# Kernel tuning notes

Hardware: AMD Instinct MI355X
Metric: run time of the kernel (lower is better)

Reference implementation:

```python
import jax, jax.numpy as jnp
import numpy as np

B, N, C = 2, 2048, 768
H = 12
HD = C // H  # 64


def setup_inputs() -> dict:
    key = jax.random.key(0)
    ks = jax.random.split(key, 6)
    s = 0.02
    x = jax.random.normal(ks[0], (B, N, C), dtype=jnp.float32)
    xpos = jnp.arange(B * N, dtype=jnp.int64).reshape(B, N) % N
    W_qkv = jax.random.normal(ks[1], (3 * C, C), dtype=jnp.float32) * s
    b_qkv = jnp.zeros((3 * C,), dtype=jnp.float32)
    W_proj = jax.random.normal(ks[2], (C, C), dtype=jnp.float32) * s
    b_proj = jnp.zeros((C,), dtype=jnp.float32)
    return {"x": x, "xpos": xpos, "W_qkv": W_qkv, "b_qkv": b_qkv,
            "W_proj": W_proj, "b_proj": b_proj}


def reference(x, xpos, W_qkv, b_qkv, W_proj, b_proj):
    # rope is None in this configuration -> xpos is unused, matching torch module.
    Bx, Nx, Cx = x.shape
    scale = (Cx // H) ** -0.5
    qkv = x @ W_qkv.T + b_qkv                     # [B, N, 3C]
    qkv = qkv.reshape(Bx, Nx, 3, H, HD)
    q = jnp.einsum('bnhd->bhnd', qkv[:, :, 0])    # [B, H, N, HD]
    k = jnp.einsum('bnhd->bhnd', qkv[:, :, 1])
    v = jnp.einsum('bnhd->bhnd', qkv[:, :, 2])
    attn = jnp.einsum('bhnd,bhmd->bhnm', q, k) * scale  # [B, H, N, N]
    attn = jax.nn.softmax(attn, axis=-1)
    out = jnp.einsum('bhnm,bhmd->bhnd', attn, v)  # [B, H, N, HD]
    out = jnp.einsum('bhnd->bnhd', out).reshape(Bx, Nx, Cx)
    return out @ W_proj.T + b_proj
```

## Files before the change

kernel.cpp:

```cpp
#include <hip/hip_runtime.h>
#include <hip/hip_bf16.h>


typedef _Float16 half8 __attribute__((ext_vector_type(8)));
typedef _Float16 half4_t __attribute__((ext_vector_type(4)));
typedef float floatx4 __attribute__((ext_vector_type(4)));
typedef float floatx16 __attribute__((ext_vector_type(16)));
typedef unsigned int uintx4 __attribute__((ext_vector_type(4)));
typedef unsigned int uintx2 __attribute__((ext_vector_type(2)));

#define SCALE_LOG2E 0.1803368801111204f

constexpr int XH_OFF    = 0;
constexpr int WQKV_OFF  = XH_OFF + 4096 * 768;
constexpr int WPROJ_OFF = WQKV_OFF + 2304 * 768;
constexpr int QK_OFF    = WPROJ_OFF + 768 * 768;
constexpr int VTH_OFF   = QK_OFF + 4096 * 1536;
constexpr int PO_OFF    = VTH_OFF + 24 * 64 * 2048;
constexpr int PSTAT_OFF = PO_OFF + 2 * 24 * 2048 * 64;

__device__ __forceinline__ void gl16(const _Float16* g, _Float16* l) {
  __builtin_amdgcn_global_load_lds(
      (const __attribute__((address_space(1))) unsigned int*)g,
      (__attribute__((address_space(3))) unsigned int*)l, 16, 0, 0);
}

__global__ __launch_bounds__(256) void cvt_all(const float* __restrict__ x,
                                               const float* __restrict__ wqkv,
                                               const float* __restrict__ wproj,
                                               _Float16* __restrict__ ws) {
  constexpr int n1 = 4096 * 768 / 4;
  constexpr int n2 = 2304 * 768 / 4;
  int i = blockIdx.x * 256 + threadIdx.x;
  const float* src; _Float16* dst; int j;
  if (i < n1)           { src = x;     dst = ws + XH_OFF;    j = i; }
  else if (i < n1 + n2) { src = wqkv;  dst = ws + WQKV_OFF;  j = i - n1; }
  else                  { src = wproj; dst = ws + WPROJ_OFF; j = i - n1 - n2; }
  floatx4 f = *(const floatx4*)(src + 4 * j);
  half4_t h;
  h[0] = (_Float16)f[0]; h[1] = (_Float16)f[1];
  h[2] = (_Float16)f[2]; h[3] = (_Float16)f[3];
  *(half4_t*)(dst + 4 * j) = h;
}

__global__ __launch_bounds__(256) void qkv_gemm(const _Float16* __restrict__ xh,
                                                const _Float16* __restrict__ wh,
                                                const float* __restrict__ bias,
                                                _Float16* __restrict__ qkh,
                                                _Float16* __restrict__ vth) {
  __shared__ __align__(16) _Float16 sA[64 * 64];
  __shared__ __align__(16) _Float16 sB[128 * 64];
  const int tid = threadIdx.x;
  const int nblk = blockIdx.x % 18, mblk = blockIdx.x / 18;
  const int lane = tid & 63, w = tid >> 6;
  const int lane15 = lane & 15, quad = lane >> 4;
  const int lrow = lane >> 3, lchunk = lane & 7;

  floatx4 acc[4][2];
#pragma unroll
  for (int mt = 0; mt < 4; ++mt)
#pragma unroll
    for (int nt = 0; nt < 2; ++nt) acc[mt][nt] = (floatx4){0.f, 0.f, 0.f, 0.f};

  for (int kt = 0; kt < 12; ++kt) {
    if (kt) __syncthreads();
#pragma unroll
    for (int i = 0; i < 6; ++i) {
      int g = w * 48 + 8 * i;
      if (g < 64)
        gl16(xh + (mblk * 64 + g + lrow) * 768 + kt * 64 + lchunk * 8, sA + g * 64);
      else
        gl16(wh + (nblk * 128 + (g - 64) + lrow) * 768 + kt * 64 + lchunk * 8,
             sB + (g - 64) * 64);
    }
    __syncthreads();
#pragma unroll
    for (int ks = 0; ks < 2; ++ks) {
      half8 af[4], bf[2];
#pragma unroll
      for (int mt = 0; mt < 4; ++mt)
        af[mt] = *(const half8*)(sA + (mt * 16 + lane15) * 64 + ks * 32 + quad * 8);
#pragma unroll
      for (int nt = 0; nt < 2; ++nt)
        bf[nt] = *(const half8*)(sB + (w * 32 + nt * 16 + lane15) * 64 + ks * 32 + quad * 8);
#pragma unroll
      for (int mt = 0; mt < 4; ++mt)
#pragma unroll
        for (int nt = 0; nt < 2; ++nt)
          acc[mt][nt] = __builtin_amdgcn_mfma_f32_16x16x32_f16(af[mt], bf[nt], acc[mt][nt], 0, 0, 0);
    }
  }

  const int mbase = mblk * 64;
#pragma unroll
  for (int nt = 0; nt < 2; ++nt) {
    int cbase = nblk * 128 + w * 32 + nt * 16;
    float bv = bias[cbase + lane15];
    if (cbase < 1536) {
      int col = cbase + lane15;
      float sc = (cbase < 768) ? SCALE_LOG2E : 1.0f;
#pragma unroll
      for (int mt = 0; mt < 4; ++mt)
#pragma unroll
        for (int r = 0; r < 4; ++r) {
          int token = mbase + mt * 16 + quad * 4 + r;
          qkh[token * 1536 + col] = (_Float16)((acc[mt][nt][r] + bv) * sc);
        }
    } else {
      int dcol = cbase - 1536 + lane15;
      int h = dcol >> 6, d = dcol & 63;
#pragma unroll
      for (int mt = 0; mt < 4; ++mt) {
        int tok0 = mbase + mt * 16 + quad * 4;
        int b = tok0 >> 11, n0 = tok0 & 2047;
        int bh = b * 12 + h;
        half4_t hv;
#pragma unroll
        for (int r = 0; r < 4; ++r) hv[r] = (_Float16)(acc[mt][nt][r] + bv);
        *(half4_t*)(vth + (bh * 64 + d) * 2048 + n0) = hv;
      }
    }
  }
}

__global__ __launch_bounds__(256, 3) void attn_fused(const _Float16* __restrict__ qkh,
                                                     const _Float16* __restrict__ vth,
                                                     _Float16* __restrict__ pO,
                                                     float* __restrict__ pL) {
  __shared__ __align__(16) _Float16 sK[2][64 * 64];
  __shared__ __align__(16) _Float16 sVT[2][64 * 64];
  const int tid = threadIdx.x;
  const int bx = blockIdx.x;
  const int bh = bx % 24;
  const int rest = bx / 24;
  const int ks = rest & 1, qt = rest >> 1;
  const int b = bh / 12, h = bh % 12;
  const int lane = tid & 63, w = tid >> 6;
  const int q = lane & 31, hi = lane >> 5;

  const int qkbase = b * 2048 * 1536 + h * 64;
  const int qrow = qt * 128 + w * 32 + q;

  half8 qf[4];
#pragma unroll
  for (int c = 0; c < 4; ++c)
    qf[c] = *(const half8*)(qkh + qkbase + qrow * 1536 + c * 16 + hi * 8);

  const int srow = tid >> 2, sc = tid & 3;
  const int key0 = ks * 1024;
  const _Float16* kp = qkh + qkbase + 768 + (key0 + srow) * 1536 + sc * 8;
  const _Float16* vp = vth + (bh * 64 + srow) * 2048 + key0 + sc * 8;
  const int sw0 = srow * 64 + ((sc ^ (srow & 7)) * 8);
  const int sw1 = srow * 64 + (((sc + 4) ^ (srow & 7)) * 8);

  floatx16 O[2];
#pragma unroll
  for (int dg = 0; dg < 2; ++dg)
#pragma unroll
    for (int i = 0; i < 16; ++i) O[dg][i] = 0.f;
  float lrow = 0.f;

  half8 rk0 = *(const half8*)kp, rk1 = *(const half8*)(kp + 32);
  half8 rv0 = *(const half8*)vp, rv1 = *(const half8*)(vp + 32);
  kp += 64 * 1536; vp += 64;
  { _Float16* nK = &sK[0][0]; _Float16* nV = &sVT[0][0];
    *(half8*)(nK + sw0) = rk0; *(half8*)(nK + sw1) = rk1;
    *(half8*)(nV + sw0) = rv0; *(half8*)(nV + sw1) = rv1; }
  rk0 = *(const half8*)kp; rk1 = *(const half8*)(kp + 32);
  rv0 = *(const half8*)vp; rv1 = *(const half8*)(vp + 32);
  kp += 64 * 1536; vp += 64;

  for (int kt = 0; kt < 16; ++kt) {
    __syncthreads();
    const _Float16* cK = &sK[kt & 1][0];
    const _Float16* cV = &sVT[kt & 1][0];
    if (kt < 15) {
      _Float16* nK = &sK[(kt + 1) & 1][0];
      _Float16* nV = &sVT[(kt + 1) & 1][0];
      *(half8*)(nK + sw0) = rk0; *(half8*)(nK + sw1) = rk1;
      *(half8*)(nV + sw0) = rv0; *(half8*)(nV + sw1) = rv1;
      if (kt < 14) {
        rk0 = *(const half8*)kp; rk1 = *(const half8*)(kp + 32);
        rv0 = *(const half8*)vp; rv1 = *(const half8*)(vp + 32);
        kp += 64 * 1536; vp += 64;
      }
    }

    floatx16 s[2];
#pragma unroll
    for (int og = 0; og < 2; ++og)
#pragma unroll
      for (int i = 0; i < 16; ++i) s[og][i] = 0.f;
#pragma unroll
    for (int c = 0; c < 4; ++c) {
      const int rc = c * 2 + hi;
#pragma unroll
      for (int og = 0; og < 2; ++og) {
        const int krow = og * 32 + q;
        half8 kf = *(const half8*)(cK + krow * 64 + ((rc ^ (krow & 7)) * 8));
        s[og] = __builtin_amdgcn_mfma_f32_32x32x16_f16(kf, qf[c], s[og], 0, 0, 0);
      }
    }

    float p[2][16];
    float rsum = 0.f;
#pragma unroll
    for (int og = 0; og < 2; ++og)
#pragma unroll
      for (int r = 0; r < 16; ++r) {
        float e = exp2f(fminf(s[og][r], 30.f));
        p[og][r] = e;
        rsum += e;
      }
    lrow += rsum;

    half8 bfrag[4];
#pragma unroll
    for (int m = 0; m < 4; ++m) {
      const int og = m >> 1, rb = (m & 1) * 8;
      unsigned ua = __builtin_bit_cast(unsigned,
          __builtin_amdgcn_cvt_pkrtz(p[og][rb + 0], p[og][rb + 1]));
      unsigned ub = __builtin_bit_cast(unsigned,
          __builtin_amdgcn_cvt_pkrtz(p[og][rb + 2], p[og][rb + 3]));
      unsigned uc = __builtin_bit_cast(unsigned,
          __builtin_amdgcn_cvt_pkrtz(p[og][rb + 4], p[og][rb + 5]));
      unsigned ud = __builtin_bit_cast(unsigned,
          __builtin_amdgcn_cvt_pkrtz(p[og][rb + 6], p[og][rb + 7]));
      uintx2 sAC = __builtin_amdgcn_permlane32_swap(ua, uc, false, false);
      uintx2 sBD = __builtin_amdgcn_permlane32_swap(ub, ud, false, false);
      uintx4 u; u[0] = sAC[0]; u[1] = sBD[0]; u[2] = sAC[1]; u[3] = sBD[1];
      bfrag[m] = __builtin_bit_cast(half8, u);
    }

#pragma unroll
    for (int m = 0; m < 4; ++m) {
      const int rc2 = m * 2 + hi;
#pragma unroll
      for (int dg = 0; dg < 2; ++dg) {
        const int vrow = dg * 32 + q;
        half8 vf = *(const half8*)(cV + vrow * 64 + ((rc2 ^ (vrow & 7)) * 8));
        O[dg] = __builtin_amdgcn_mfma_f32_32x32x16_f16(vf, bfrag[m], O[dg], 0, 0, 0);
      }
    }
  }

  const int prow = (ks * 24 + bh) * 2048 + qt * 128 + w * 32;
#pragma unroll
  for (int dg = 0; dg < 2; ++dg)
#pragma unroll
    for (int g2 = 0; g2 < 4; ++g2) {
      half4_t hv;
#pragma unroll
      for (int e = 0; e < 4; ++e) hv[e] = (_Float16)O[dg][g2 * 4 + e];
      *(half4_t*)(pO + (prow + q) * 64 + dg * 32 + g2 * 8 + hi * 4) = hv;
    }
  lrow += __shfl_xor(lrow, 32, 64);
  if (lane < 32) pL[prow + lane] = lrow;
}

__global__ __launch_bounds__(256) void proj_gemm(const _Float16* __restrict__ pO,
                                                 const float* __restrict__ pL,
                                                 const _Float16* __restrict__ wh,
                                                 const float* __restrict__ bias,
                                                 float* __restrict__ out) {
  __shared__ __align__(16) _Float16 sA[64 * 72];
  __shared__ __align__(16) _Float16 sB[128 * 64];
  const int tid = threadIdx.x;
  const int nblk = blockIdx.x % 6, mblk = blockIdx.x / 6;
  const int lane = tid & 63, w = tid >> 6;
  const int lane15 = lane & 15, quad = lane >> 4;
  const int lrow = lane >> 3, lchunk = lane & 7;
  const int arow = tid >> 2, achk = tid & 3;
  const int tok0 = mblk * 64;
  const int b = tok0 >> 11, tokl = tok0 & 2047;

  floatx4 acc[4][2];
#pragma unroll
  for (int mt = 0; mt < 4; ++mt)
#pragma unroll
    for (int nt = 0; nt < 2; ++nt) acc[mt][nt] = (floatx4){0.f, 0.f, 0.f, 0.f};

  for (int kt = 0; kt < 12; ++kt) {
    const int bh = b * 12 + kt;
    const int row1 = bh * 2048 + tokl + arow;
    const int row2 = (24 + bh) * 2048 + tokl + arow;
    float f = 1.0f / (pL[row1] + pL[row2]);

    if (kt) __syncthreads();
#pragma unroll
    for (int i = 0; i < 4; ++i) {
      int g = w * 32 + 8 * i;
      gl16(wh + (nblk * 128 + g + lrow) * 768 + kt * 64 + lchunk * 8, sB + g * 64);
    }
#pragma unroll
    for (int cc = 0; cc < 2; ++cc) {
      int c8 = achk + 4 * cc;
      half8 o1 = *(const half8*)(pO + row1 * 64 + c8 * 8);
      half8 o2 = *(const half8*)(pO + row2 * 64 + c8 * 8);
      half8 o;
#pragma unroll
      for (int e = 0; e < 8; ++e)
        o[e] = (_Float16)(f * ((float)o1[e] + (float)o2[e]));
      *(half8*)(sA + arow * 72 + c8 * 8) = o;
    }
    __syncthreads();

#pragma unroll
    for (int ksplit = 0; ksplit < 2; ++ksplit) {
      half8 af[4], bf[2];
#pragma unroll
      for (int mt = 0; mt < 4; ++mt)
        af[mt] = *(const half8*)(sA + (mt * 16 + lane15) * 72 + ksplit * 32 + quad * 8);
#pragma unroll
      for (int nt = 0; nt < 2; ++nt)
        bf[nt] = *(const half8*)(sB + (w * 32 + nt * 16 + lane15) * 64 + ksplit * 32 + quad * 8);
#pragma unroll
      for (int mt = 0; mt < 4; ++mt)
#pragma unroll
        for (int nt = 0; nt < 2; ++nt)
          acc[mt][nt] = __builtin_amdgcn_mfma_f32_16x16x32_f16(af[mt], bf[nt], acc[mt][nt], 0, 0, 0);
    }
  }

  const int mbase = mblk * 64;
#pragma unroll
  for (int nt = 0; nt < 2; ++nt) {
    int col = nblk * 128 + w * 32 + nt * 16 + lane15;
    float bv = bias[col];
#pragma unroll
    for (int mt = 0; mt < 4; ++mt)
#pragma unroll
      for (int r = 0; r < 4; ++r) {
        int token = mbase + mt * 16 + quad * 4 + r;
        out[token * 768 + col] = acc[mt][nt][r] + bv;
      }
  }
}

extern "C" void kernel_launch(void* const* d_in, const int* in_sizes, int n_in,
                              void* d_out, int out_size, void* d_ws, size_t ws_size,
                              hipStream_t stream) {
  const float* x     = (const float*)d_in[0];
  const float* wqkv  = (const float*)d_in[2];
  const float* bqkv  = (const float*)d_in[3];
  const float* wproj = (const float*)d_in[4];
  const float* bproj = (const float*)d_in[5];
  float* out = (float*)d_out;

  _Float16* ws = (_Float16*)d_ws;
  _Float16* xh     = ws + XH_OFF;
  _Float16* wqkvh  = ws + WQKV_OFF;
  _Float16* wprojh = ws + WPROJ_OFF;
  _Float16* qkh    = ws + QK_OFF;
  _Float16* vth    = ws + VTH_OFF;
  _Float16* pO     = ws + PO_OFF;
  float*    pL     = (float*)(ws + PSTAT_OFF);

  constexpr int total_v4 = (4096 * 768 + 2304 * 768 + 768 * 768) / 4;
  cvt_all<<<total_v4 / 256, 256, 0, stream>>>(x, wqkv, wproj, ws);
  qkv_gemm<<<64 * 18, 256, 0, stream>>>(xh, wqkvh, bqkv, qkh, vth);
  attn_fused<<<24 * 32, 256, 0, stream>>>(qkh, vth, pO, pL);
  proj_gemm<<<64 * 6, 256, 0, stream>>>(pO, pL, wprojh, bproj, out);
}
```

Before: 183.0 us.

## Split attention keys four ways and enlarge QKV GEMM tiles to 128x128

The attention kernel is templated on the number of key splits. When the workspace is large enough it uses four key segments instead of two, doubling the block count to 1536 for better occupancy across CUs, and the projection GEMM sums all partial outputs and row sums. Separately, the QKV GEMM tile grows from 64x128 to 128x128, with each warp computing a 64x64 sub-tile, for more reuse per LDS load and fewer blocks. The costs are more partial-output traffic and merge work in the projection, and higher register pressure in the QKV GEMM.

```diff
diff --git a/kernel.cpp b/kernel.cpp
--- a/kernel.cpp
+++ b/kernel.cpp
@@ -17,7 +17,8 @@
 constexpr int QK_OFF    = WPROJ_OFF + 768 * 768;
 constexpr int VTH_OFF   = QK_OFF + 4096 * 1536;
 constexpr int PO_OFF    = VTH_OFF + 24 * 64 * 2048;
-constexpr int PSTAT_OFF = PO_OFF + 2 * 24 * 2048 * 64;
+constexpr size_t WS4_BYTES =
+    ((size_t)PO_OFF + (size_t)4 * 24 * 2048 * 64 + (size_t)4 * 24 * 2048 * 2) * 2;
 
 __device__ __forceinline__ void gl16(const _Float16* g, _Float16* l) {
   __builtin_amdgcn_global_load_lds(
@@ -48,53 +49,54 @@
                                                 const float* __restrict__ bias,
                                                 _Float16* __restrict__ qkh,
                                                 _Float16* __restrict__ vth) {
-  __shared__ __align__(16) _Float16 sA[64 * 64];
+  __shared__ __align__(16) _Float16 sA[128 * 64];
   __shared__ __align__(16) _Float16 sB[128 * 64];
   const int tid = threadIdx.x;
   const int nblk = blockIdx.x % 18, mblk = blockIdx.x / 18;
   const int lane = tid & 63, w = tid >> 6;
   const int lane15 = lane & 15, quad = lane >> 4;
   const int lrow = lane >> 3, lchunk = lane & 7;
-
-  floatx4 acc[4][2];
+  const int wq = w >> 1, wn = w & 1;
+
+  floatx4 acc[4][4];
 #pragma unroll
   for (int mt = 0; mt < 4; ++mt)
 #pragma unroll
-    for (int nt = 0; nt < 2; ++nt) acc[mt][nt] = (floatx4){0.f, 0.f, 0.f, 0.f};
+    for (int nt = 0; nt < 4; ++nt) acc[mt][nt] = (floatx4){0.f, 0.f, 0.f, 0.f};
 
   for (int kt = 0; kt < 12; ++kt) {
     if (kt) __syncthreads();
 #pragma unroll
-    for (int i = 0; i < 6; ++i) {
-      int g = w * 48 + 8 * i;
-      if (g < 64)
-        gl16(xh + (mblk * 64 + g + lrow) * 768 + kt * 64 + lchunk * 8, sA + g * 64);
+    for (int i = 0; i < 8; ++i) {
+      int g = i * 32 + w * 8;
+      if (g < 128)
+        gl16(xh + (mblk * 128 + g + lrow) * 768 + kt * 64 + lchunk * 8, sA + g * 64);
       else
-        gl16(wh + (nblk * 128 + (g - 64) + lrow) * 768 + kt * 64 + lchunk * 8,
-             sB + (g - 64) * 64);
+        gl16(wh + (nblk * 128 + (g - 128) + lrow) * 768 + kt * 64 + lchunk * 8,
+             sB + (g - 128) * 64);
     }
     __syncthreads();
 #pragma unroll
     for (int ks = 0; ks < 2; ++ks) {
-      half8 af[4], bf[2];
-#pragma unroll
-      for (int mt = 0; mt < 4; ++mt)
-        af[mt] = *(const half8*)(sA + (mt * 16 + lane15) * 64 + ks * 32 + quad * 8);
-#pragma unroll
-      for (int nt = 0; nt < 2; ++nt)
-        bf[nt] = *(const half8*)(sB + (w * 32 + nt * 16 + lane15) * 64 + ks * 32 + quad * 8);
-#pragma unroll
-      for (int mt = 0; mt < 4; ++mt)
-#pragma unroll
-        for (int nt = 0; nt < 2; ++nt)
+      half8 af[4], bf[4];
+#pragma unroll
+      for (int mt = 0; mt < 4; ++mt)
+        af[mt] = *(const half8*)(sA + (wq * 64 + mt * 16 + lane15) * 64 + ks * 32 + quad * 8);
+#pragma unroll
+      for (int nt = 0; nt < 4; ++nt)
+        bf[nt] = *(const half8*)(sB + (wn * 64 + nt * 16 + lane15) * 64 + ks * 32 + quad * 8);
+#pragma unroll
+      for (int mt = 0; mt < 4; ++mt)
+#pragma unroll
+        for (int nt = 0; nt < 4; ++nt)
           acc[mt][nt] = __builtin_amdgcn_mfma_f32_16x16x32_f16(af[mt], bf[nt], acc[mt][nt], 0, 0, 0);
     }
   }
 
-  const int mbase = mblk * 64;
-#pragma unroll
-  for (int nt = 0; nt < 2; ++nt) {
-    int cbase = nblk * 128 + w * 32 + nt * 16;
+  const int mbase = mblk * 128 + wq * 64;
+#pragma unroll
+  for (int nt = 0; nt < 4; ++nt) {
+    int cbase = nblk * 128 + wn * 64 + nt * 16;
     float bv = bias[cbase + lane15];
     if (cbase < 1536) {
       int col = cbase + lane15;
@@ -123,17 +125,20 @@
   }
 }
 
+template <int NKS>
 __global__ __launch_bounds__(256, 3) void attn_fused(const _Float16* __restrict__ qkh,
                                                      const _Float16* __restrict__ vth,
                                                      _Float16* __restrict__ pO,
                                                      float* __restrict__ pL) {
+  constexpr int SEG = 2048 / NKS;
+  constexpr int NT = SEG / 64;
   __shared__ __align__(16) _Float16 sK[2][64 * 64];
   __shared__ __align__(16) _Float16 sVT[2][64 * 64];
   const int tid = threadIdx.x;
   const int bx = blockIdx.x;
   const int bh = bx % 24;
   const int rest = bx / 24;
-  const int ks = rest & 1, qt = rest >> 1;
+  const int ks = rest % NKS, qt = rest / NKS;
   const int b = bh / 12, h = bh % 12;
   const int lane = tid & 63, w = tid >> 6;
   const int q = lane & 31, hi = lane >> 5;
@@ -147,7 +152,7 @@
     qf[c] = *(const half8*)(qkh + qkbase + qrow * 1536 + c * 16 + hi * 8);
 
   const int srow = tid >> 2, sc = tid & 3;
-  const int key0 = ks * 1024;
+  const int key0 = ks * SEG;
   const _Float16* kp = qkh + qkbase + 768 + (key0 + srow) * 1536 + sc * 8;
   const _Float16* vp = vth + (bh * 64 + srow) * 2048 + key0 + sc * 8;
   const int sw0 = srow * 64 + ((sc ^ (srow & 7)) * 8);
@@ -170,16 +175,16 @@
   rv0 = *(const half8*)vp; rv1 = *(const half8*)(vp + 32);
   kp += 64 * 1536; vp += 64;
 
-  for (int kt = 0; kt < 16; ++kt) {
+  for (int kt = 0; kt < NT; ++kt) {
     __syncthreads();
     const _Float16* cK = &sK[kt & 1][0];
     const _Float16* cV = &sVT[kt & 1][0];
-    if (kt < 15) {
+    if (kt < NT - 1) {
       _Float16* nK = &sK[(kt + 1) & 1][0];
       _Float16* nV = &sVT[(kt + 1) & 1][0];
       *(half8*)(nK + sw0) = rk0; *(half8*)(nK + sw1) = rk1;
       *(half8*)(nV + sw0) = rv0; *(half8*)(nV + sw1) = rv1;
-      if (kt < 14) {
+      if (kt < NT - 2) {
         rk0 = *(const half8*)kp; rk1 = *(const half8*)(kp + 32);
         rv0 = *(const half8*)vp; rv1 = *(const half8*)(vp + 32);
         kp += 64 * 1536; vp += 64;
@@ -258,6 +263,7 @@
   if (lane < 32) pL[prow + lane] = lrow;
 }
 
+template <int NKS>
 __global__ __launch_bounds__(256) void proj_gemm(const _Float16* __restrict__ pO,
                                                  const float* __restrict__ pL,
                                                  const _Float16* __restrict__ wh,
@@ -282,9 +288,11 @@
 
   for (int kt = 0; kt < 12; ++kt) {
     const int bh = b * 12 + kt;
-    const int row1 = bh * 2048 + tokl + arow;
-    const int row2 = (24 + bh) * 2048 + tokl + arow;
-    float f = 1.0f / (pL[row1] + pL[row2]);
+    float ls = 0.f;
+#pragma unroll
+    for (int s = 0; s < NKS; ++s)
+      ls += pL[(s * 24 + bh) * 2048 + tokl + arow];
+    float f = 1.0f / ls;
 
     if (kt) __syncthreads();
 #pragma unroll
@@ -295,13 +303,17 @@
 #pragma unroll
     for (int cc = 0; cc < 2; ++cc) {
       int c8 = achk + 4 * cc;
-      half8 o1 = *(const half8*)(pO + row1 * 64 + c8 * 8);
-      half8 o2 = *(const half8*)(pO + row2 * 64 + c8 * 8);
-      half8 o;
-#pragma unroll
-      for (int e = 0; e < 8; ++e)
-        o[e] = (_Float16)(f * ((float)o1[e] + (float)o2[e]));
-      *(half8*)(sA + arow * 72 + c8 * 8) = o;
+      float fo[8] = {0.f, 0.f, 0.f, 0.f, 0.f, 0.f, 0.f, 0.f};
+#pragma unroll
+      for (int s = 0; s < NKS; ++s) {
+        half8 o = *(const half8*)(pO + ((s * 24 + bh) * 2048 + tokl + arow) * 64 + c8 * 8);
+#pragma unroll
+        for (int e = 0; e < 8; ++e) fo[e] += (float)o[e];
+      }
+      half8 oo;
+#pragma unroll
+      for (int e = 0; e < 8; ++e) oo[e] = (_Float16)(f * fo[e]);
+      *(half8*)(sA + arow * 72 + c8 * 8) = oo;
     }
     __syncthreads();
 
@@ -354,11 +366,18 @@
   _Float16* qkh    = ws + QK_OFF;
   _Float16* vth    = ws + VTH_OFF;
   _Float16* pO     = ws + PO_OFF;
-  float*    pL     = (float*)(ws + PSTAT_OFF);
 
   constexpr int total_v4 = (4096 * 768 + 2304 * 768 + 768 * 768) / 4;
   cvt_all<<<total_v4 / 256, 256, 0, stream>>>(x, wqkv, wproj, ws);
-  qkv_gemm<<<64 * 18, 256, 0, stream>>>(xh, wqkvh, bqkv, qkh, vth);
-  attn_fused<<<24 * 32, 256, 0, stream>>>(qkh, vth, pO, pL);
-  proj_gemm<<<64 * 6, 256, 0, stream>>>(pO, pL, wprojh, bproj, out);
-}
+  qkv_gemm<<<32 * 18, 256, 0, stream>>>(xh, wqkvh, bqkv, qkh, vth);
+
+  if (ws_size >= WS4_BYTES) {
+    float* pL = (float*)(ws + PO_OFF + 4 * 24 * 2048 * 64);
+    attn_fused<4><<<24 * 64, 256, 0, stream>>>(qkh, vth, pO, pL);
+    proj_gemm<4><<<64 * 6, 256, 0, stream>>>(pO, pL, wprojh, bproj, out);
+  } else {
+    float* pL = (float*)(ws + PO_OFF + 2 * 24 * 2048 * 64);
+    attn_fused<2><<<24 * 32, 256, 0, stream>>>(qkh, vth, pO, pL);
+    proj_gemm<2><<<64 * 6, 256, 0, stream>>>(pO, pL, wprojh, bproj, out);
+  }
+}
```

Measured after the change: 189.7 us. 3.7% more time.

## Enlarge QKV GEMM tile to 128x128 and interleave softmax with PV MFMAs

Applied to the files above, without the earlier changes.

The QKV projection GEMM now uses 128x128 block tiles with a 2x2 wave layout, giving each wave a 64x64 sub-tile. This halves the grid and raises fragment reuse per LDS load. The attention inner loop is restructured so each 32-key score group is computed, exponentiated with the raw hardware exp2, packed, and fed straight into the PV MFMAs. This shortens register live ranges and lets exp work overlap with matrix ops. The clamp at 30 before exp2 is dropped, so any score above that limit is no longer bounded and could overflow fp16 P values.

```diff
diff --git a/kernel.cpp b/kernel.cpp
--- a/kernel.cpp
+++ b/kernel.cpp
@@ -48,53 +48,54 @@
                                                 const float* __restrict__ bias,
                                                 _Float16* __restrict__ qkh,
                                                 _Float16* __restrict__ vth) {
-  __shared__ __align__(16) _Float16 sA[64 * 64];
+  __shared__ __align__(16) _Float16 sA[128 * 64];
   __shared__ __align__(16) _Float16 sB[128 * 64];
   const int tid = threadIdx.x;
   const int nblk = blockIdx.x % 18, mblk = blockIdx.x / 18;
   const int lane = tid & 63, w = tid >> 6;
   const int lane15 = lane & 15, quad = lane >> 4;
   const int lrow = lane >> 3, lchunk = lane & 7;
-
-  floatx4 acc[4][2];
+  const int wq = w >> 1, wn = w & 1;
+
+  floatx4 acc[4][4];
 #pragma unroll
   for (int mt = 0; mt < 4; ++mt)
 #pragma unroll
-    for (int nt = 0; nt < 2; ++nt) acc[mt][nt] = (floatx4){0.f, 0.f, 0.f, 0.f};
+    for (int nt = 0; nt < 4; ++nt) acc[mt][nt] = (floatx4){0.f, 0.f, 0.f, 0.f};
 
   for (int kt = 0; kt < 12; ++kt) {
     if (kt) __syncthreads();
 #pragma unroll
-    for (int i = 0; i < 6; ++i) {
-      int g = w * 48 + 8 * i;
-      if (g < 64)
-        gl16(xh + (mblk * 64 + g + lrow) * 768 + kt * 64 + lchunk * 8, sA + g * 64);
+    for (int i = 0; i < 8; ++i) {
+      int g = i * 32 + w * 8;
+      if (g < 128)
+        gl16(xh + (mblk * 128 + g + lrow) * 768 + kt * 64 + lchunk * 8, sA + g * 64);
       else
-        gl16(wh + (nblk * 128 + (g - 64) + lrow) * 768 + kt * 64 + lchunk * 8,
-             sB + (g - 64) * 64);
+        gl16(wh + (nblk * 128 + (g - 128) + lrow) * 768 + kt * 64 + lchunk * 8,
+             sB + (g - 128) * 64);
     }
     __syncthreads();
 #pragma unroll
     for (int ks = 0; ks < 2; ++ks) {
-      half8 af[4], bf[2];
-#pragma unroll
-      for (int mt = 0; mt < 4; ++mt)
-        af[mt] = *(const half8*)(sA + (mt * 16 + lane15) * 64 + ks * 32 + quad * 8);
-#pragma unroll
-      for (int nt = 0; nt < 2; ++nt)
-        bf[nt] = *(const half8*)(sB + (w * 32 + nt * 16 + lane15) * 64 + ks * 32 + quad * 8);
-#pragma unroll
-      for (int mt = 0; mt < 4; ++mt)
-#pragma unroll
-        for (int nt = 0; nt < 2; ++nt)
+      half8 af[4], bf[4];
+#pragma unroll
+      for (int mt = 0; mt < 4; ++mt)
+        af[mt] = *(const half8*)(sA + (wq * 64 + mt * 16 + lane15) * 64 + ks * 32 + quad * 8);
+#pragma unroll
+      for (int nt = 0; nt < 4; ++nt)
+        bf[nt] = *(const half8*)(sB + (wn * 64 + nt * 16 + lane15) * 64 + ks * 32 + quad * 8);
+#pragma unroll
+      for (int mt = 0; mt < 4; ++mt)
+#pragma unroll
+        for (int nt = 0; nt < 4; ++nt)
           acc[mt][nt] = __builtin_amdgcn_mfma_f32_16x16x32_f16(af[mt], bf[nt], acc[mt][nt], 0, 0, 0);
     }
   }
 
-  const int mbase = mblk * 64;
-#pragma unroll
-  for (int nt = 0; nt < 2; ++nt) {
-    int cbase = nblk * 128 + w * 32 + nt * 16;
+  const int mbase = mblk * 128 + wq * 64;
+#pragma unroll
+  for (int nt = 0; nt < 4; ++nt) {
+    int cbase = nblk * 128 + wn * 64 + nt * 16;
     float bv = bias[cbase + lane15];
     if (cbase < 1536) {
       int col = cbase + lane15;
@@ -186,62 +187,50 @@
       }
     }
 
-    floatx16 s[2];
-#pragma unroll
-    for (int og = 0; og < 2; ++og)
-#pragma unroll
-      for (int i = 0; i < 16; ++i) s[og][i] = 0.f;
-#pragma unroll
-    for (int c = 0; c < 4; ++c) {
-      const int rc = c * 2 + hi;
-#pragma unroll
-      for (int og = 0; og < 2; ++og) {
-        const int krow = og * 32 + q;
-        half8 kf = *(const half8*)(cK + krow * 64 + ((rc ^ (krow & 7)) * 8));
-        s[og] = __builtin_amdgcn_mfma_f32_32x32x16_f16(kf, qf[c], s[og], 0, 0, 0);
-      }
-    }
-
-    float p[2][16];
     float rsum = 0.f;
 #pragma unroll
-    for (int og = 0; og < 2; ++og)
-#pragma unroll
-      for (int r = 0; r < 16; ++r) {
-        float e = exp2f(fminf(s[og][r], 30.f));
-        p[og][r] = e;
-        rsum += e;
-      }
+    for (int og = 0; og < 2; ++og) {
+      floatx16 s;
+#pragma unroll
+      for (int i = 0; i < 16; ++i) s[i] = 0.f;
+      const int krow = og * 32 + q;
+#pragma unroll
+      for (int c = 0; c < 4; ++c) {
+        half8 kf = *(const half8*)(cK + krow * 64 + (((c * 2 + hi) ^ (krow & 7)) * 8));
+        s = __builtin_amdgcn_mfma_f32_32x32x16_f16(kf, qf[c], s, 0, 0, 0);
+      }
+
+#pragma unroll
+      for (int mm = 0; mm < 2; ++mm) {
+        const int rb = mm * 8;
+        float e0 = __builtin_amdgcn_exp2f(s[rb + 0]);
+        float e1 = __builtin_amdgcn_exp2f(s[rb + 1]);
+        float e2 = __builtin_amdgcn_exp2f(s[rb + 2]);
+        float e3 = __builtin_amdgcn_exp2f(s[rb + 3]);
+        float e4 = __builtin_amdgcn_exp2f(s[rb + 4]);
+        float e5 = __builtin_amdgcn_exp2f(s[rb + 5]);
+        float e6 = __builtin_amdgcn_exp2f(s[rb + 6]);
+        float e7 = __builtin_amdgcn_exp2f(s[rb + 7]);
+        rsum += ((e0 + e1) + (e2 + e3)) + ((e4 + e5) + (e6 + e7));
+        unsigned ua = __builtin_bit_cast(unsigned, __builtin_amdgcn_cvt_pkrtz(e0, e1));
+        unsigned ub = __builtin_bit_cast(unsigned, __builtin_amdgcn_cvt_pkrtz(e2, e3));
+        unsigned uc = __builtin_bit_cast(unsigned, __builtin_amdgcn_cvt_pkrtz(e4, e5));
+        unsigned ud = __builtin_bit_cast(unsigned, __builtin_amdgcn_cvt_pkrtz(e6, e7));
+        uintx2 sAC = __builtin_amdgcn_permlane32_swap(ua, uc, false, false);
+        uintx2 sBD = __builtin_amdgcn_permlane32_swap(ub, ud, false, false);
+        uintx4 u; u[0] = sAC[0]; u[1] = sBD[0]; u[2] = sAC[1]; u[3] = sBD[1];
+        half8 bfrag = __builtin_bit_cast(half8, u);
+
+        const int rc2 = (og * 2 + mm) * 2 + hi;
+#pragma unroll
+        for (int dg = 0; dg < 2; ++dg) {
+          const int vrow = dg * 32 + q;
+          half8 vf = *(const half8*)(cV + vrow * 64 + ((rc2 ^ (vrow & 7)) * 8));
+          O[dg] = __builtin_amdgcn_mfma_f32_32x32x16_f16(vf, bfrag, O[dg], 0, 0, 0);
+        }
+      }
+    }
     lrow += rsum;
-
-    half8 bfrag[4];
-#pragma unroll
-    for (int m = 0; m < 4; ++m) {
-      const int og = m >> 1, rb = (m & 1) * 8;
-      unsigned ua = __builtin_bit_cast(unsigned,
-          __builtin_amdgcn_cvt_pkrtz(p[og][rb + 0], p[og][rb + 1]));
-      unsigned ub = __builtin_bit_cast(unsigned,
-          __builtin_amdgcn_cvt_pkrtz(p[og][rb + 2], p[og][rb + 3]));
-      unsigned uc = __builtin_bit_cast(unsigned,
-          __builtin_amdgcn_cvt_pkrtz(p[og][rb + 4], p[og][rb + 5]));
-      unsigned ud = __builtin_bit_cast(unsigned,
-          __builtin_amdgcn_cvt_pkrtz(p[og][rb + 6], p[og][rb + 7]));
-      uintx2 sAC = __builtin_amdgcn_permlane32_swap(ua, uc, false, false);
-      uintx2 sBD = __builtin_amdgcn_permlane32_swap(ub, ud, false, false);
-      uintx4 u; u[0] = sAC[0]; u[1] = sBD[0]; u[2] = sAC[1]; u[3] = sBD[1];
-      bfrag[m] = __builtin_bit_cast(half8, u);
-    }
-
-#pragma unroll
-    for (int m = 0; m < 4; ++m) {
-      const int rc2 = m * 2 + hi;
-#pragma unroll
-      for (int dg = 0; dg < 2; ++dg) {
-        const int vrow = dg * 32 + q;
-        half8 vf = *(const half8*)(cV + vrow * 64 + ((rc2 ^ (vrow & 7)) * 8));
-        O[dg] = __builtin_amdgcn_mfma_f32_32x32x16_f16(vf, bfrag[m], O[dg], 0, 0, 0);
-      }
-    }
   }
 
   const int prow = (ks * 24 + bh) * 2048 + qt * 128 + w * 32;
@@ -358,7 +347,7 @@
 
   constexpr int total_v4 = (4096 * 768 + 2304 * 768 + 768 * 768) / 4;
   cvt_all<<<total_v4 / 256, 256, 0, stream>>>(x, wqkv, wproj, ws);
-  qkv_gemm<<<64 * 18, 256, 0, stream>>>(xh, wqkvh, bqkv, qkh, vth);
+  qkv_gemm<<<32 * 18, 256, 0, stream>>>(xh, wqkvh, bqkv, qkh, vth);
   attn_fused<<<24 * 32, 256, 0, stream>>>(qkh, vth, pO, pL);
   proj_gemm<<<64 * 6, 256, 0, stream>>>(pO, pL, wprojh, bproj, out);
 }
```

Result: faster. 161.2 us, median of 2 (-11.9%).
